# Kernel tuning notes

Hardware: AMD Instinct MI355X
Metric: run time of the kernel (lower is better)

## Reference

```python
import jax, jax.numpy as jnp
import numpy as np

MAX_DISP = 40   # corr(40,1,40,1,1): max horizontal displacement (stereo disparity)
SLOPE = 0.1     # LeakyReLU negative slope


def _compress(x, W, b):
    # 3x3 conv, stride 1, pad 1 (NCHW), then LeakyReLU(0.1)
    y = jax.lax.conv_general_dilated(
        x, W, window_strides=(1, 1), padding=((1, 1), (1, 1)),
        dimension_numbers=('NCHW', 'OIHW', 'NCHW'))
    y = y + b[None, :, None, None]
    return jnp.where(y >= 0, y, SLOPE * y)


def _corr1d(a, b):
    # 1-D horizontal correlation (DispNetC style): for disparity d in [0, MAX_DISP],
    # corr[:, d, y, x] = mean_c a[:, c, y, x] * b[:, c, y, x - d], zero-padded.
    B, C, H, Wd = a.shape
    bp = jnp.pad(b, ((0, 0), (0, 0), (0, 0), (MAX_DISP, 0)))
    outs = [
        jnp.mean(a * jax.lax.dynamic_slice_in_dim(bp, MAX_DISP - d, Wd, axis=3), axis=1)
        for d in range(MAX_DISP + 1)
    ]  # small fixed loop over 41 displacements
    return jnp.stack(outs, axis=1)  # [B, 41, H, W]


def setup_inputs() -> dict:
    key = jax.random.key(0)
    k1, k2, k3 = jax.random.split(key, 3)
    B, C, H, W = 8, 64, 192, 384
    conv1a = jax.random.normal(k1, (B, C, H, W), dtype=jnp.float32)
    conv1b = jax.random.normal(k2, (B, C, H, W), dtype=jnp.float32)
    W_comp = jax.random.normal(k3, (16, 64, 3, 3), dtype=jnp.float32) * 0.05
    b_comp = jnp.zeros((16,), dtype=jnp.float32)
    return {"conv1a": conv1a, "conv1b": conv1b, "W_comp": W_comp, "b_comp": b_comp}


def reference(conv1a, conv1b, W_comp, b_comp):
    a_mini = _compress(conv1a, W_comp, b_comp)  # [B,16,H,W]
    b_mini = _compress(conv1b, W_comp, b_comp)  # shared weights, as in the module
    return _corr1d(a_mini, b_mini)              # [B,41,H,W]
```

## Files before the change

kernel.cpp:

```cpp
#include <hip/hip_runtime.h>
#include <hip/hip_bf16.h>

#define B_   8
#define CIN  64
#define CM   16
#define H_   192
#define W_   384
#define ND   41
#define HW   (H_ * W_)
#define SLOPE 0.1f
#define SMINI ((size_t)B_ * CM * H_ * W_)

typedef __attribute__((ext_vector_type(8))) short short8v;
typedef __attribute__((ext_vector_type(4))) float floatx4;

__device__ __forceinline__ float bf2f(short h) {
    union { unsigned u; float f; } cv;
    cv.u = ((unsigned)(unsigned short)h) << 16;
    return cv.f;
}
__device__ __forceinline__ short f2bf(float f) {
    __hip_bfloat16 h = __float2bfloat16(f);
    return *(short*)&h;
}

__global__ void wprep_kernel(const float* __restrict__ w, short* __restrict__ wbf) {
    int i = blockIdx.x * 256 + threadIdx.x;
    if (i >= CM * 576) return;
    int co = i / 576, k = i - co * 576;
    int t = k >> 6, c = k & 63;
    wbf[i] = f2bf(w[(co * CIN + c) * 9 + t]);
}

#define YT 6
#define XT 32
#define LC 34
#define PSTR 72

__global__ __launch_bounds__(256, 4) void conv_mfma(
    const float* __restrict__ ina, const float* __restrict__ inb,
    const short* __restrict__ wbf, const float* __restrict__ bias,
    short* __restrict__ mini)
{
    __shared__ __align__(16) short px[8 * LC * PSTR];

    int blk = blockIdx.x;
    int xt = blk % 12;  blk /= 12;
    int yt = blk % 32;  blk /= 32;
    int b  = blk & 7;
    int t  = blk >> 3;
    const float* src = t ? inb : ina;
    int x0 = xt * XT, y0 = yt * YT;
    int tid = threadIdx.x;

    int t4 = tid >> 4;
    int cq = tid & 15;
    int c0 = cq << 2;
    floatx4 v[5][4];
    int wbase_[5], lxb_[5];
    bool vld[5];
    #pragma unroll
    for (int i = 0; i < 5; ++i) {
        int g = i * 16 + t4;
        int xq = g % 10;
        int row = g / 10;
        int gy = y0 - 1 + row;
        int gx = x0 - 4 + xq * 4;
        bool ok = ((unsigned)gy < (unsigned)H_) && ((unsigned)gx < (unsigned)W_);
        vld[i] = ok;
        int lxb = gx - x0 + 1;
        lxb_[i] = lxb;
        wbase_[i] = (row * LC + lxb) * PSTR + c0;
        int gyc = ok ? gy : 0;
        int gxc = ok ? gx : 0;
        const float* p = src + (size_t)(b * CIN + c0) * HW
                       + (size_t)gyc * W_ + gxc;
        v[i][0] = *(const floatx4*)p;
        v[i][1] = *(const floatx4*)(p + HW);
        v[i][2] = *(const floatx4*)(p + 2 * HW);
        v[i][3] = *(const floatx4*)(p + 3 * HW);
    }

    #pragma unroll
    for (int i = 0; i < 5; ++i) {
        #pragma unroll
        for (int j = 0; j < 4; ++j) {
            if ((unsigned)(lxb_[i] + j) < (unsigned)LC) {
                float f0 = vld[i] ? v[i][0][j] : 0.f;
                float f1 = vld[i] ? v[i][1][j] : 0.f;
                float f2 = vld[i] ? v[i][2][j] : 0.f;
                float f3 = vld[i] ? v[i][3][j] : 0.f;
                short4 q;
                q.x = f2bf(f0); q.y = f2bf(f1);
                q.z = f2bf(f2); q.w = f2bf(f3);
                *(short4*)(px + wbase_[i] + j * PSTR) = q;
            }
        }
    }

    int lane = tid & 63;
    int n16  = lane & 15;
    int quad = lane >> 4;

    short8v af[18];
    #pragma unroll
    for (int ks = 0; ks < 18; ++ks)
        af[ks] = *(const short8v*)(wbf + n16 * 576 + ks * 32 + quad * 8);

    __syncthreads();

    int wv = tid >> 6;
    floatx4 acc[3] = {{0,0,0,0},{0,0,0,0},{0,0,0,0}};
    int base[3];
    #pragma unroll
    for (int j = 0; j < 3; ++j) {
        int mt = wv * 3 + j;
        int r = mt >> 1, xb = (mt & 1) << 4;
        base[j] = (r * LC + xb + n16) * PSTR + quad * 8;
    }
    #pragma unroll
    for (int ks = 0; ks < 18; ++ks) {
        const int tap = ks >> 1, ch = ks & 1;
        const int dy = tap / 3, dx = tap % 3;
        const int off = (dy * LC + dx) * PSTR + ch * 32;
        #pragma unroll
        for (int j = 0; j < 3; ++j) {
            short8v bfr = *(const short8v*)(px + base[j] + off);
            acc[j] = __builtin_amdgcn_mfma_f32_16x16x32_bf16(af[ks], bfr, acc[j], 0, 0, 0);
        }
    }

    float bia[4];
    #pragma unroll
    for (int i = 0; i < 4; ++i) bia[i] = bias[quad * 4 + i];
    #pragma unroll
    for (int j = 0; j < 3; ++j) {
        int mt = wv * 3 + j;
        int r = mt >> 1, xb = (mt & 1) << 4;
        int y = y0 + r, x = x0 + xb + n16;
        size_t o = (((size_t)(t * B_ + b) * H_ + y) * W_ + x) * CM + quad * 4;
        short4 q;
        float v2;
        v2 = acc[j][0] + bia[0]; v2 = v2 >= 0.f ? v2 : SLOPE * v2; q.x = f2bf(v2);
        v2 = acc[j][1] + bia[1]; v2 = v2 >= 0.f ? v2 : SLOPE * v2; q.y = f2bf(v2);
        v2 = acc[j][2] + bia[2]; v2 = v2 >= 0.f ? v2 : SLOPE * v2; q.z = f2bf(v2);
        v2 = acc[j][3] + bia[3]; v2 = v2 >= 0.f ? v2 : SLOPE * v2; q.w = f2bf(v2);
        *(short4*)(mini + o) = q;
    }
}

#define BSTR 24

__global__ __launch_bounds__(384) void corr_nhwc(
    const short* __restrict__ mini, float* __restrict__ out)
{
    __shared__ __align__(16) short bl[W_ * BSTR];
    int b = blockIdx.x / H_;
    int y = blockIdx.x % H_;
    int x = threadIdx.x;

    size_t arow = ((size_t)b * H_ + y) * W_ * CM;
    size_t brow = ((size_t)(B_ + b) * H_ + y) * W_ * CM;

    short8v p0 = *(const short8v*)(mini + brow + (size_t)x * CM);
    short8v p1 = *(const short8v*)(mini + brow + (size_t)x * CM + 8);
    *(short8v*)(bl + x * BSTR) = p0;
    *(short8v*)(bl + x * BSTR + 8) = p1;

    float av[16];
    short8v a0 = *(const short8v*)(mini + arow + (size_t)x * CM);
    short8v a1 = *(const short8v*)(mini + arow + (size_t)x * CM + 8);
    #pragma unroll
    for (int i = 0; i < 8; ++i) { av[i] = bf2f(a0[i]); av[8 + i] = bf2f(a1[i]); }

    __syncthreads();

    float* ob = out + ((size_t)b * ND * H_ + y) * W_ + x;
    #pragma unroll 1
    for (int d = 0; d < ND; ++d) {
        float s = 0.f;
        int xs = x - d;
        if (xs >= 0) {
            const short* bp = bl + xs * BSTR;
            short8v c0 = *(const short8v*)bp;
            short8v c1 = *(const short8v*)(bp + 8);
            float s0 = 0.f, s1 = 0.f;
            #pragma unroll
            for (int i = 0; i < 8; ++i) {
                s0 += av[i]     * bf2f(c0[i]);
                s1 += av[8 + i] * bf2f(c1[i]);
            }
            s = s0 + s1;
        }
        ob[(size_t)d * HW] = s * 0.0625f;
    }
}

extern "C" void kernel_launch(void* const* d_in, const int* in_sizes, int n_in,
                              void* d_out, int out_size, void* d_ws, size_t ws_size,
                              hipStream_t stream) {
    const float* conv1a = (const float*)d_in[0];
    const float* conv1b = (const float*)d_in[1];
    const float* W_comp = (const float*)d_in[2];
    const float* b_comp = (const float*)d_in[3];
    float* out = (float*)d_out;

    short* mini = (short*)d_ws;
    short* wbf  = mini + 2 * SMINI;

    wprep_kernel<<<36, 256, 0, stream>>>(W_comp, wbf);
    conv_mfma<<<2 * B_ * 32 * 12, 256, 0, stream>>>(conv1a, conv1b, wbf, b_comp, mini);
    corr_nhwc<<<B_ * H_, 384, 0, stream>>>(mini, out);
}
```

Before: 441.0 us.

## Pre-transpose inputs to NHWC bf16 and stage conv tiles via direct global-to-LDS loads

A new transpose kernel converts both fp32 NCHW inputs into a bf16 NHWC buffer in workspace. A new conv kernel then fills its LDS tile with global_load_lds DMA, using an XOR swizzle against bank conflicts, and zero-fills only edge tiles. The old fused conv is kept as a fallback when workspace is too small. This adds an extra full write and read of a roughly 150MB intermediate in exchange for simpler, coalesced tile loads in the conv.

New measurement: 449.3 us. Within noise of the previous version (+1.9%).

```diff
diff --git a/kernel.cpp b/kernel.cpp
--- a/kernel.cpp
+++ b/kernel.cpp
@@ -24,6 +24,12 @@
     return *(short*)&h;
 }
 
+__device__ __forceinline__ void gload_lds16(const void* g, void* l) {
+    __builtin_amdgcn_global_load_lds(
+        (const __attribute__((address_space(1))) void*)g,
+        (__attribute__((address_space(3))) void*)l, 16, 0, 0);
+}
+
 __global__ void wprep_kernel(const float* __restrict__ w, short* __restrict__ wbf) {
     int i = blockIdx.x * 256 + threadIdx.x;
     if (i >= CM * 576) return;
@@ -32,8 +38,147 @@
     wbf[i] = f2bf(w[(co * CIN + c) * 9 + t]);
 }
 
-#define YT 6
-#define XT 32
+#define TXW  192
+#define TSTR 72
+
+__global__ __launch_bounds__(256) void txp_kernel(
+    const float* __restrict__ ina, const float* __restrict__ inb,
+    short* __restrict__ xT)
+{
+    __shared__ __align__(16) short xl[TXW * TSTR];
+    int blk = blockIdx.x;
+    blk = (blk & 7) * (gridDim.x >> 3) + (blk >> 3);
+    int xh = blk & 1;  blk >>= 1;
+    int y  = blk % H_; blk /= H_;
+    int b  = blk & 7;
+    int t  = blk >> 3;
+    const float* src = t ? inb : ina;
+    int tid = threadIdx.x;
+
+    #pragma unroll
+    for (int i = 0; i < 12; ++i) {
+        int e = i * 256 + tid;
+        int xq = e % 48;
+        int c  = e / 48;
+        floatx4 v = *(const floatx4*)(src + (size_t)(b * CIN + c) * HW
+                                      + (size_t)y * W_ + xh * TXW + xq * 4);
+        int x4 = xq * 4;
+        xl[(x4 + 0) * TSTR + c] = f2bf(v[0]);
+        xl[(x4 + 1) * TSTR + c] = f2bf(v[1]);
+        xl[(x4 + 2) * TSTR + c] = f2bf(v[2]);
+        xl[(x4 + 3) * TSTR + c] = f2bf(v[3]);
+    }
+    __syncthreads();
+
+    size_t obase = (((size_t)(t * B_ + b) * H_ + y) * W_ + xh * TXW) * 64;
+    #pragma unroll
+    for (int i = 0; i < 6; ++i) {
+        int e = i * 256 + tid;
+        int cg = e & 7, x = e >> 3;
+        short8v q = *(const short8v*)(xl + x * TSTR + cg * 8);
+        *(short8v*)(xT + obase + (size_t)x * 64 + cg * 8) = q;
+    }
+}
+
+__global__ __launch_bounds__(256, 4) void conv_dma(
+    const short* __restrict__ xT, const short* __restrict__ wbf,
+    const float* __restrict__ bias, short* __restrict__ mini)
+{
+    __shared__ __align__(16) short px[272 * 64];
+    int blk = blockIdx.x;
+    blk = (blk & 7) * (gridDim.x >> 3) + (blk >> 3);
+    int xt = blk % 12;  blk /= 12;
+    int yt = blk % 32;  blk /= 32;
+    int b  = blk & 7;
+    int t  = blk >> 3;
+    int x0 = xt * 32, y0 = yt * 6;
+    int tid  = threadIdx.x;
+    int lane = tid & 63, wv = tid >> 6;
+
+    const char* xTb = (const char*)xT;
+    char* pxb = (char*)px;
+    size_t pbase = (size_t)(t * B_ + b) * H_ * W_;
+
+    bool edge = (yt == 0) | (yt == 31) | (xt == 0) | (xt == 11);
+    if (edge) {
+        #pragma unroll
+        for (int i = 0; i < 17; ++i)
+            *(unsigned long long*)(pxb + (i * 256 + tid) * 8) = 0ull;
+        __syncthreads();
+    }
+
+    int sub = lane >> 3;
+    int opc = (lane & 7) << 4;
+    auto issue = [&](int k) {
+        int s   = k * 8 + sub;
+        int row = (s * 241) >> 13;
+        int lx  = s - row * 34;
+        int gy  = y0 - 1 + row, gx = x0 - 1 + lx;
+        int o   = opc ^ ((s & 3) << 4);
+        const char* gp = xTb + ((pbase + (size_t)gy * W_ + gx) * 128 + o);
+        void* lp = pxb + k * 1024;
+        if (!edge) {
+            gload_lds16(gp, lp);
+        } else if (((unsigned)gy < (unsigned)H_) & ((unsigned)gx < (unsigned)W_)) {
+            gload_lds16(gp, lp);
+        }
+    };
+    #pragma unroll
+    for (int i = 0; i < 8; ++i) issue(wv * 8 + i);
+    if (wv < 2) issue(32 + wv);
+
+    int n16 = lane & 15, quad = lane >> 4;
+    short8v af[18];
+    #pragma unroll
+    for (int ks = 0; ks < 18; ++ks)
+        af[ks] = *(const short8v*)(wbf + n16 * 576 + ks * 32 + quad * 8);
+
+    __syncthreads();
+
+    floatx4 acc[3] = {{0,0,0,0},{0,0,0,0},{0,0,0,0}};
+    int base128[3];
+    int Zj[3][4];
+    #pragma unroll
+    for (int j = 0; j < 3; ++j) {
+        int mt = wv * 3 + j;
+        int r = mt >> 1, xb = (mt & 1) << 4;
+        base128[j] = (r * 34 + xb + n16) * 128;
+        #pragma unroll
+        for (int m = 0; m < 4; ++m)
+            Zj[j][m] = (quad << 4) ^ (((2 * r + n16 + m) & 3) << 4);
+    }
+    #pragma unroll
+    for (int ks = 0; ks < 18; ++ks) {
+        const int tap = ks >> 1, ch = ks & 1;
+        const int dy = tap / 3, dx = tap % 3;
+        const int d = dy * 34 + dx;
+        #pragma unroll
+        for (int j = 0; j < 3; ++j) {
+            short8v bfr = *(const short8v*)(pxb + base128[j] + Zj[j][d & 3]
+                                            + (d * 128 + ch * 64));
+            acc[j] = __builtin_amdgcn_mfma_f32_16x16x32_bf16(af[ks], bfr, acc[j], 0, 0, 0);
+        }
+    }
+
+    float bia[4];
+    #pragma unroll
+    for (int i = 0; i < 4; ++i) bia[i] = bias[quad * 4 + i];
+    #pragma unroll
+    for (int j = 0; j < 3; ++j) {
+        int mt = wv * 3 + j;
+        int r = mt >> 1, xb = (mt & 1) << 4;
+        int y = y0 + r, x = x0 + xb + n16;
+        size_t o = (((size_t)(t * B_ + b) * H_ + y) * W_ + x) * CM + quad * 4;
+        short4 q;
+        float v2;
+        v2 = acc[j][0] + bia[0]; v2 = v2 >= 0.f ? v2 : SLOPE * v2; q.x = f2bf(v2);
+        v2 = acc[j][1] + bia[1]; v2 = v2 >= 0.f ? v2 : SLOPE * v2; q.y = f2bf(v2);
+        v2 = acc[j][2] + bia[2]; v2 = v2 >= 0.f ? v2 : SLOPE * v2; q.z = f2bf(v2);
+        v2 = acc[j][3] + bia[3]; v2 = v2 >= 0.f ? v2 : SLOPE * v2; q.w = f2bf(v2);
+        *(short4*)(mini + o) = q;
+    }
+}
+
 #define LC 34
 #define PSTR 72
 
@@ -42,15 +187,14 @@
     const short* __restrict__ wbf, const float* __restrict__ bias,
     short* __restrict__ mini)
 {
-    __shared__ __align__(16) short px[8 * LC * PSTR];
-
+    __shared__ __align__(16) short pxl[8 * LC * PSTR];
     int blk = blockIdx.x;
     int xt = blk % 12;  blk /= 12;
     int yt = blk % 32;  blk /= 32;
     int b  = blk & 7;
     int t  = blk >> 3;
     const float* src = t ? inb : ina;
-    int x0 = xt * XT, y0 = yt * YT;
+    int x0 = xt * 32, y0 = yt * 6;
     int tid = threadIdx.x;
 
     int t4 = tid >> 4;
@@ -73,14 +217,12 @@
         wbase_[i] = (row * LC + lxb) * PSTR + c0;
         int gyc = ok ? gy : 0;
         int gxc = ok ? gx : 0;
-        const float* p = src + (size_t)(b * CIN + c0) * HW
-                       + (size_t)gyc * W_ + gxc;
+        const float* p = src + (size_t)(b * CIN + c0) * HW + (size_t)gyc * W_ + gxc;
         v[i][0] = *(const floatx4*)p;
         v[i][1] = *(const floatx4*)(p + HW);
         v[i][2] = *(const floatx4*)(p + 2 * HW);
         v[i][3] = *(const floatx4*)(p + 3 * HW);
     }
-
     #pragma unroll
     for (int i = 0; i < 5; ++i) {
         #pragma unroll
@@ -93,22 +235,18 @@
                 short4 q;
                 q.x = f2bf(f0); q.y = f2bf(f1);
                 q.z = f2bf(f2); q.w = f2bf(f3);
-                *(short4*)(px + wbase_[i] + j * PSTR) = q;
+                *(short4*)(pxl + wbase_[i] + j * PSTR) = q;
             }
         }
     }
-
     int lane = tid & 63;
     int n16  = lane & 15;
     int quad = lane >> 4;
-
     short8v af[18];
     #pragma unroll
     for (int ks = 0; ks < 18; ++ks)
         af[ks] = *(const short8v*)(wbf + n16 * 576 + ks * 32 + quad * 8);
-
     __syncthreads();
-
     int wv = tid >> 6;
     floatx4 acc[3] = {{0,0,0,0},{0,0,0,0},{0,0,0,0}};
     int base[3];
@@ -125,11 +263,10 @@
         const int off = (dy * LC + dx) * PSTR + ch * 32;
         #pragma unroll
         for (int j = 0; j < 3; ++j) {
-            short8v bfr = *(const short8v*)(px + base[j] + off);
+            short8v bfr = *(const short8v*)(pxl + base[j] + off);
             acc[j] = __builtin_amdgcn_mfma_f32_16x16x32_bf16(af[ks], bfr, acc[j], 0, 0, 0);
         }
     }
-
     float bia[4];
     #pragma unroll
     for (int i = 0; i < 4; ++i) bia[i] = bias[quad * 4 + i];
@@ -207,8 +344,15 @@
 
     short* mini = (short*)d_ws;
     short* wbf  = mini + 2 * SMINI;
+    short* xT   = wbf + 9216;
+    const size_t need = 37748736ull + 18432ull + 150994944ull;
 
     wprep_kernel<<<36, 256, 0, stream>>>(W_comp, wbf);
-    conv_mfma<<<2 * B_ * 32 * 12, 256, 0, stream>>>(conv1a, conv1b, wbf, b_comp, mini);
+    if (ws_size >= need) {
+        txp_kernel<<<6144, 256, 0, stream>>>(conv1a, conv1b, xT);
+        conv_dma<<<6144, 256, 0, stream>>>(xT, wbf, b_comp, mini);
+    } else {
+        conv_mfma<<<6144, 256, 0, stream>>>(conv1a, conv1b, wbf, b_comp, mini);
+    }
     corr_nhwc<<<B_ * H_, 384, 0, stream>>>(mini, out);
 }
```
